# Kernel optimization log

Measured on AMD Instinct MI355X. Metric: run time of the kernel, lower is better.

## Reference

```python
import jax, jax.numpy as jnp
import numpy as np

IN_CH = 64
OUT_CH = 64
SEQ_LEN = 2048
MODES = 64  # modes2 = min(modes1, seq_len//2) = 64
SCALE = 1.0 / (IN_CH * OUT_CH)


def setup_inputs() -> dict:
    key = jax.random.key(0)
    k1, k2, k3 = jax.random.split(key, 3)
    x = jax.random.normal(k1, (32, 8, IN_CH, SEQ_LEN), dtype=jnp.float32)
    # torch.rand(...) complex init scaled by 1/(in*out): real & imag in [0, scale)
    wr = SCALE * jax.random.uniform(k2, (IN_CH, OUT_CH, MODES), dtype=jnp.float32)
    wi = SCALE * jax.random.uniform(k3, (IN_CH, OUT_CH, MODES), dtype=jnp.float32)
    return {"x": x, "wr": wr, "wi": wi}


def reference(x, wr, wi):
    # x: [B, H, E, N] real; weights complex [in, out, modes]
    N = x.shape[-1]
    w = jax.lax.complex(wr, wi)
    x_ft = jnp.fft.rfft(x)                       # [B, H, E, N//2+1] complex64
    a = x_ft[..., :MODES]                        # keep only low modes
    out_low = jnp.einsum('bjix,iox->bjox', a, w)  # per-mode complex matmul
    # zero-fill remaining frequency bins (equivalent to out_ft zeros + slice set)
    pad = N // 2 + 1 - MODES
    out_ft = jnp.pad(out_low, ((0, 0), (0, 0), (0, 0), (0, pad)))
    return jnp.fft.irfft(out_ft, n=N)            # [B, H, out_ch, N] real
```

## Files before the change

### kernel.cpp

```cpp
#include <hip/hip_runtime.h>
#include <hip/hip_bf16.h>


typedef __bf16 bf16x8 __attribute__((ext_vector_type(8)));
typedef float  f32x4  __attribute__((ext_vector_type(4)));

#define SEQ 2048
#define NM2 128
#define KS  2

__device__ __forceinline__ unsigned int rnbf(float f) {
  unsigned int u = __builtin_bit_cast(unsigned int, f);
  return (u + 0x7fffu + ((u >> 16) & 1u)) >> 16;
}
__device__ __forceinline__ unsigned int pack2(float a, float b) {
  return rnbf(a) | (rnbf(b) << 16);
}
__device__ __forceinline__ float frombf(unsigned int lo16_in_place) {
  return __builtin_bit_cast(float, lo16_in_place);
}

typedef const __attribute__((address_space(1))) unsigned int gu32;
typedef __attribute__((address_space(3))) unsigned int lu32;

__global__ __launch_bounds__(256) void k_tables(unsigned short* __restrict__ t1sw,
                                                unsigned short* __restrict__ t2t) {
  int idx = blockIdx.x * 256 + threadIdx.x;
  int k = idx >> 11;
  int n = idx & 2047;
  float rev = (float)((k * n) & 2047) * (1.0f / 2048.0f);
  float s, co;
  asm("v_sin_f32 %0, %1" : "=v"(s)  : "v"(rev));
  asm("v_cos_f32 %0, %1" : "=v"(co) : "v"(rev));
  float ck = (k == 0 ? 1.0f : 2.0f) * (1.0f / 2048.0f);
  int kt = n >> 6, part = (n >> 3) & 7, e = n & 7;
  unsigned base = (unsigned)kt * 16384u + 2u * (unsigned)e;
  unsigned offc = base + (((unsigned)(k * 128 + part * 16)) ^ (((unsigned)k & 7u) << 4));
  int c2 = k + 64;
  unsigned offs = base + (((unsigned)(c2 * 128 + part * 16)) ^ (((unsigned)c2 & 7u) << 4));
  *(unsigned short*)((char*)t1sw + offc) = (unsigned short)rnbf(co);
  *(unsigned short*)((char*)t1sw + offs) = (unsigned short)rnbf(-s);
  t2t[n * NM2 + k]      = (unsigned short)rnbf(ck * co);
  t2t[n * NM2 + k + 64] = (unsigned short)rnbf(-ck * s);
}

__global__ __launch_bounds__(256) void k_gemm1(const float* __restrict__ x,
                                               const unsigned short* __restrict__ t1sw,
                                               unsigned short* __restrict__ P) {
  __shared__ int4 lds4[81920 / 16];
  char* lds = (char*)lds4;
  const int tid = threadIdx.x, wave = tid >> 6, lane = tid & 63;
  const int mtile = blockIdx.x >> 1, ks = blockIdx.x & (KS - 1);
  const int r0 = mtile * 64;
  const int kbase = ks * (SEQ / KS);
  const char* t1base = (const char*)t1sw + (size_t)(kbase >> 6) * 16384;

  const float* xsrc[4];
#pragma unroll
  for (int p = 0; p < 4; ++p) {
    const int row = p * 16 + wave * 4 + (lane >> 4);
    const int u = (lane & 15) ^ (row & 7);
    xsrc[p] = x + (size_t)(r0 + row) * SEQ + kbase + u * 4;
  }

#define STAGE_X(t, buf)                                                              \
  {                                                                                  \
    _Pragma("unroll")                                                                \
    for (int p = 0; p < 4; ++p)                                                      \
      __builtin_amdgcn_global_load_lds((gu32*)(xsrc[p] + (t) * 64),                  \
          (lu32*)(lds + (buf) * 16384 + p * 4096 + wave * 1024), 16, 0, 0);          \
  }
#define STAGE_T(t, buf)                                                              \
  {                                                                                  \
    const char* tg_ = t1base + (size_t)(t) * 16384;                                  \
    _Pragma("unroll")                                                                \
    for (int p = 0; p < 4; ++p)                                                      \
      __builtin_amdgcn_global_load_lds((gu32*)(tg_ + (p * 256 + tid) * 16),          \
          (lu32*)(lds + 49152 + (buf) * 16384 + p * 4096 + wave * 1024), 16, 0, 0);  \
  }

  f32x4 acc[8] = {};

  STAGE_T(0, 0);
  STAGE_X(0, 0);
  STAGE_X(1, 1);

  const int a = wave * 16 + (lane & 15);
  const unsigned xra = (unsigned)(a & 7) << 4;
  const int kg = lane >> 4;

  for (int it = 0; it < 16; ++it) {
    asm volatile("s_waitcnt vmcnt(4)" ::: "memory");
    __builtin_amdgcn_s_barrier();
    {
      const int tn = (it + 1 < 16) ? it + 1 : 15;
      const int xn = (it + 2 < 16) ? it + 2 : 15;
      STAGE_T(tn, (it + 1) & 1);
      STAGE_X(xn, (it + 2) % 3);
    }
    const int xoff = (it % 3) * 16384;
    const int toff = 49152 + (it & 1) * 16384;
#pragma unroll
    for (int kss = 0; kss < 2; ++kss) {
      const unsigned byte0 = (unsigned)(a * 256 + kss * 128 + kg * 32);
      const f32x4 lo = *(const f32x4*)(lds + xoff + (byte0 ^ xra));
      const f32x4 hi = *(const f32x4*)(lds + xoff + ((byte0 + 16) ^ xra));
      unsigned c0, c1, c2, c3;
      asm("v_cvt_pk_bf16_f32 %0, %1, %2" : "=v"(c0) : "v"(lo[0]), "v"(lo[1]));
      asm("v_cvt_pk_bf16_f32 %0, %1, %2" : "=v"(c1) : "v"(lo[2]), "v"(lo[3]));
      asm("v_cvt_pk_bf16_f32 %0, %1, %2" : "=v"(c2) : "v"(hi[0]), "v"(hi[1]));
      asm("v_cvt_pk_bf16_f32 %0, %1, %2" : "=v"(c3) : "v"(hi[2]), "v"(hi[3]));
      uint4 pk; pk.x = c0; pk.y = c1; pk.z = c2; pk.w = c3;
      const bf16x8 av = __builtin_bit_cast(bf16x8, pk);
#pragma unroll
      for (int t = 0; t < 8; ++t) {
        const int col = t * 16 + (lane & 15);
        const bf16x8 bv = *(const bf16x8*)(lds + toff +
            ((col * 128 + kss * 64 + kg * 16) ^ ((unsigned)(col & 7) << 4)));
        acc[t] = __builtin_amdgcn_mfma_f32_16x16x32_bf16(bv, av, acc[t], 0, 0, 0);
      }
    }
  }
  unsigned short* Pout = P + (size_t)ks * (16384 * NM2);
  const int row = r0 + wave * 16 + (lane & 15);
#pragma unroll
  for (int t = 0; t < 8; ++t) {
    const int col0 = t * 16 + kg * 4;
    uint2 v; v.x = pack2(acc[t][0], acc[t][1]); v.y = pack2(acc[t][2], acc[t][3]);
    *(uint2*)(Pout + (size_t)row * NM2 + col0) = v;
  }
#undef STAGE_X
#undef STAGE_T
}

__global__ __launch_bounds__(256) void k_stage2(const unsigned short* __restrict__ P,
                                                const float* __restrict__ wr,
                                                const float* __restrict__ wi,
                                                unsigned short* __restrict__ Bx) {
  __shared__ float sA[2][64][64];
  const int b = blockIdx.x;
  const int bjc = b >> 2, oh = (b >> 1) & 1, kh = b & 1;
  const int k0 = kh * 32;
  const int tid = threadIdx.x;
#pragma unroll
  for (int p = 0; p < 8; ++p) {
    int fidx = tid + 256 * p;
    int row = fidx >> 4, q = fidx & 15;
    int colbf = (q < 8) ? (k0 + q * 4) : (64 + k0 + (q - 8) * 4);
    const unsigned short* base = P + (size_t)(bjc * 128 + row) * NM2 + colbf;
    uint2 u0 = *(const uint2*)(base);
    uint2 u1 = *(const uint2*)(base + (size_t)16384 * NM2);
    f32x4 v;
    v[0] = frombf(u0.x << 16)         + frombf(u1.x << 16);
    v[1] = frombf(u0.x & 0xffff0000u) + frombf(u1.x & 0xffff0000u);
    v[2] = frombf(u0.y << 16)         + frombf(u1.y << 16);
    v[3] = frombf(u0.y & 0xffff0000u) + frombf(u1.y & 0xffff0000u);
    int dcol = (q < 8) ? q * 4 : 32 + (q - 8) * 4;
    *(f32x4*)(&sA[row >> 6][row & 63][dcol]) = v;
  }
  __syncthreads();
  const int o = oh * 32 + (tid >> 3);
  const int kg = tid & 7;
  const int kb = k0 + kg * 4;
  f32x4 accr[2] = {};
  f32x4 acci[2] = {};
  for (int i = 0; i < 64; ++i) {
    f32x4 wrv = *(const f32x4*)(wr + (i * 64 + o) * 64 + kb);
    f32x4 wiv = *(const f32x4*)(wi + (i * 64 + o) * 64 + kb);
#pragma unroll
    for (int bj = 0; bj < 2; ++bj) {
      f32x4 ar = *(const f32x4*)(&sA[bj][i][kg * 4]);
      f32x4 ai = *(const f32x4*)(&sA[bj][i][32 + kg * 4]);
#pragma unroll
      for (int kk = 0; kk < 4; ++kk) {
        accr[bj][kk] += ar[kk] * wrv[kk] - ai[kk] * wiv[kk];
        acci[bj][kk] += ar[kk] * wiv[kk] + ai[kk] * wrv[kk];
      }
    }
  }
#pragma unroll
  for (int bj = 0; bj < 2; ++bj) {
    const int r = (bjc * 2 + bj) * 64 + o;
    uint2 vr; vr.x = pack2(accr[bj][0], accr[bj][1]); vr.y = pack2(accr[bj][2], accr[bj][3]);
    uint2 vi; vi.x = pack2(acci[bj][0], acci[bj][1]); vi.y = pack2(acci[bj][2], acci[bj][3]);
    *(uint2*)(Bx + (size_t)r * NM2 + kb)      = vr;
    *(uint2*)(Bx + (size_t)r * NM2 + 64 + kb) = vi;
  }
}

__global__ __launch_bounds__(256) void k_gemm2(const unsigned short* __restrict__ Bx,
                                               const unsigned short* __restrict__ t2t,
                                               float* __restrict__ out) {
  __shared__ int4 lds4[65536 / 16];
  char* lds = (char*)lds4;
  const int tid = threadIdx.x, wave = tid >> 6, lane = tid & 63;
  const int swz = (blockIdx.x & 7) * 256 + (blockIdx.x >> 3);
  const int mb = swz >> 4, nb = swz & 15;
  const int r0 = mb * 128, n0 = nb * 128;
#pragma unroll
  for (int p = 0; p < 8; ++p) {
    int seg = tid + 256 * p;
    int row = seg >> 4, part = seg & 15;
    unsigned sw = (unsigned)((row * 256 + part * 16) ^ ((row & 7) << 4));
    int4 va = *(const int4*)(Bx + (size_t)(r0 + row) * NM2 + part * 8);
    *(int4*)(lds + sw) = va;
    int4 vb = *(const int4*)(t2t + (size_t)(n0 + row) * NM2 + part * 8);
    *(int4*)(lds + 32768 + sw) = vb;
  }
  __syncthreads();
  f32x4 acc[2][8] = {};
#pragma unroll
  for (int ks = 0; ks < 4; ++ks) {
    const int ar0 = wave * 32 + (lane & 15);
    const int ar1 = ar0 + 16;
    const int koff = ks * 64 + (lane >> 4) * 16;
    bf16x8 a0 = *(const bf16x8*)(lds + ((ar0 * 256 + koff) ^ ((unsigned)(ar0 & 7) << 4)));
    bf16x8 a1 = *(const bf16x8*)(lds + ((ar1 * 256 + koff) ^ ((unsigned)(ar1 & 7) << 4)));
#pragma unroll
    for (int t = 0; t < 8; ++t) {
      const int col = t * 16 + (lane & 15);
      bf16x8 bv = *(const bf16x8*)(lds + 32768 + ((col * 256 + koff) ^ ((unsigned)(col & 7) << 4)));
      acc[0][t] = __builtin_amdgcn_mfma_f32_16x16x32_bf16(bv, a0, acc[0][t], 0, 0, 0);
      acc[1][t] = __builtin_amdgcn_mfma_f32_16x16x32_bf16(bv, a1, acc[1][t], 0, 0, 0);
    }
  }
#pragma unroll
  for (int m = 0; m < 2; ++m) {
    const int row = r0 + wave * 32 + m * 16 + (lane & 15);
#pragma unroll
    for (int t = 0; t < 8; ++t) {
      const int col = n0 + t * 16 + (lane >> 4) * 4;
      *(f32x4*)(out + (size_t)row * SEQ + col) = acc[m][t];
    }
  }
}

extern "C" void kernel_launch(void* const* d_in, const int* in_sizes, int n_in,
                              void* d_out, int out_size, void* d_ws, size_t ws_size,
                              hipStream_t stream) {
  const float* x  = (const float*)d_in[0];
  const float* wr = (const float*)d_in[1];
  const float* wi = (const float*)d_in[2];
  float* out = (float*)d_out;
  char* ws = (char*)d_ws;
  unsigned short* t1sw = (unsigned short*)(ws);
  unsigned short* t2t  = (unsigned short*)(ws + 524288);
  unsigned short* P    = (unsigned short*)(ws + 1048576);
  unsigned short* Bx   = (unsigned short*)(ws + 1048576 + (size_t)KS * 16384 * NM2 * 2);

  k_tables<<<dim3(512),      dim3(256), 0, stream>>>(t1sw, t2t);
  k_gemm1 <<<dim3(256 * KS), dim3(256), 0, stream>>>(x, t1sw, P);
  k_stage2<<<dim3(512),      dim3(256), 0, stream>>>(P, wr, wi, Bx);
  k_gemm2 <<<dim3(2048),     dim3(256), 0, stream>>>(Bx, t2t, out);
}
```

Measured before the change: 99.01 us.

## Switch gemm1 to double-buffered LDS pipeline and use nontemporal output stores

The first GEMM kernel drops its triple-buffered x / double-buffered table staging with a two-deep prefetch and vmcnt(4) partial waits. It moves to a simple double buffer that prefetches one tile ahead and waits for all loads plus a barrier at the end of each iteration. This cuts LDS from 80KB to 64KB per block, which may allow more resident blocks, but exposes more load latency because each iteration fully drains. Separately, the final kernel writes its fp32 output with nontemporal stores to avoid polluting cache.

```diff
diff --git a/kernel.cpp b/kernel.cpp
--- a/kernel.cpp
+++ b/kernel.cpp
@@ -47,7 +47,7 @@
 __global__ __launch_bounds__(256) void k_gemm1(const float* __restrict__ x,
                                                const unsigned short* __restrict__ t1sw,
                                                unsigned short* __restrict__ P) {
-  __shared__ int4 lds4[81920 / 16];
+  __shared__ int4 lds4[65536 / 16];
   char* lds = (char*)lds4;
   const int tid = threadIdx.x, wave = tid >> 6, lane = tid & 63;
   const int mtile = blockIdx.x >> 1, ks = blockIdx.x & (KS - 1);
@@ -63,43 +63,40 @@
     xsrc[p] = x + (size_t)(r0 + row) * SEQ + kbase + u * 4;
   }
 
-#define STAGE_X(t, buf)                                                              \
-  {                                                                                  \
-    _Pragma("unroll")                                                                \
-    for (int p = 0; p < 4; ++p)                                                      \
-      __builtin_amdgcn_global_load_lds((gu32*)(xsrc[p] + (t) * 64),                  \
-          (lu32*)(lds + (buf) * 16384 + p * 4096 + wave * 1024), 16, 0, 0);          \
-  }
-#define STAGE_T(t, buf)                                                              \
-  {                                                                                  \
-    const char* tg_ = t1base + (size_t)(t) * 16384;                                  \
-    _Pragma("unroll")                                                                \
-    for (int p = 0; p < 4; ++p)                                                      \
-      __builtin_amdgcn_global_load_lds((gu32*)(tg_ + (p * 256 + tid) * 16),          \
-          (lu32*)(lds + 49152 + (buf) * 16384 + p * 4096 + wave * 1024), 16, 0, 0);  \
-  }
-
   f32x4 acc[8] = {};
 
-  STAGE_T(0, 0);
-  STAGE_X(0, 0);
-  STAGE_X(1, 1);
+#pragma unroll
+  for (int p = 0; p < 4; ++p)
+    __builtin_amdgcn_global_load_lds((gu32*)(xsrc[p]),
+                                     (lu32*)(lds + p * 4096 + wave * 1024), 16, 0, 0);
+#pragma unroll
+  for (int p = 0; p < 4; ++p)
+    __builtin_amdgcn_global_load_lds((gu32*)(t1base + (p * 256 + tid) * 16),
+                                     (lu32*)(lds + 32768 + (p * 256 + wave * 64) * 16), 16, 0, 0);
+  asm volatile("s_waitcnt vmcnt(0)" ::: "memory");
+  __builtin_amdgcn_s_barrier();
 
   const int a = wave * 16 + (lane & 15);
   const unsigned xra = (unsigned)(a & 7) << 4;
   const int kg = lane >> 4;
 
   for (int it = 0; it < 16; ++it) {
-    asm volatile("s_waitcnt vmcnt(4)" ::: "memory");
-    __builtin_amdgcn_s_barrier();
-    {
-      const int tn = (it + 1 < 16) ? it + 1 : 15;
-      const int xn = (it + 2 < 16) ? it + 2 : 15;
-      STAGE_T(tn, (it + 1) & 1);
-      STAGE_X(xn, (it + 2) % 3);
-    }
-    const int xoff = (it % 3) * 16384;
-    const int toff = 49152 + (it & 1) * 16384;
+    const int cur = it & 1, nxt = cur ^ 1;
+    const int xoff = cur * 16384;
+    const int toff = 32768 + cur * 16384;
+    if (it < 15) {
+      const char* tg = t1base + (size_t)(it + 1) * 16384;
+#pragma unroll
+      for (int p = 0; p < 4; ++p)
+        __builtin_amdgcn_global_load_lds((gu32*)(xsrc[p] + (it + 1) * 64),
+                                         (lu32*)(lds + nxt * 16384 + p * 4096 + wave * 1024),
+                                         16, 0, 0);
+#pragma unroll
+      for (int p = 0; p < 4; ++p)
+        __builtin_amdgcn_global_load_lds((gu32*)(tg + (p * 256 + tid) * 16),
+                                         (lu32*)(lds + 32768 + nxt * 16384 + (p * 256 + wave * 64) * 16),
+                                         16, 0, 0);
+    }
 #pragma unroll
     for (int kss = 0; kss < 2; ++kss) {
       const unsigned byte0 = (unsigned)(a * 256 + kss * 128 + kg * 32);
@@ -120,6 +117,8 @@
         acc[t] = __builtin_amdgcn_mfma_f32_16x16x32_bf16(bv, av, acc[t], 0, 0, 0);
       }
     }
+    asm volatile("s_waitcnt vmcnt(0)" ::: "memory");
+    __builtin_amdgcn_s_barrier();
   }
   unsigned short* Pout = P + (size_t)ks * (16384 * NM2);
   const int row = r0 + wave * 16 + (lane & 15);
@@ -129,8 +128,6 @@
     uint2 v; v.x = pack2(acc[t][0], acc[t][1]); v.y = pack2(acc[t][2], acc[t][3]);
     *(uint2*)(Pout + (size_t)row * NM2 + col0) = v;
   }
-#undef STAGE_X
-#undef STAGE_T
 }
 
 __global__ __launch_bounds__(256) void k_stage2(const unsigned short* __restrict__ P,
@@ -230,7 +227,7 @@
 #pragma unroll
     for (int t = 0; t < 8; ++t) {
       const int col = n0 + t * 16 + (lane >> 4) * 4;
-      *(f32x4*)(out + (size_t)row * SEQ + col) = acc[m][t];
+      __builtin_nontemporal_store(acc[m][t], (f32x4*)(out + (size_t)row * SEQ + col));
     }
   }
 }
```

Measured after the change: 99.07 us. No clear change (+0.1%).
